# Performance work log

Hardware: AMD Instinct MI355X
Metric: run time of the kernel (lower is better)

The kernel has to match this reference:

```python
import jax, jax.numpy as jnp
import numpy as np

B, S, D_MODEL, N_HEADS = 2, 2048, 1024, 16
HEAD_DIM = D_MODEL // N_HEADS
BASE = 10000.0

# 3D RoPE slice sizes: n_pairs = head_dim//2 split into x,y,z
_n_pairs = HEAD_DIM // 2
_px = _n_pairs // 3
_py = _n_pairs // 3
_pz = _n_pairs - _px - _py
D_X, D_Y, D_Z = _px * 2, _py * 2, _pz * 2  # 20, 20, 24


def _rotate_half(x):
    # interleaved pairs: (x0,x1,x2,x3,...) -> (-x1,x0,-x3,x2,...)
    x1 = x[..., ::2]
    x2 = x[..., 1::2]
    return jnp.stack((-x2, x1), axis=-1).reshape(x.shape)


def _rope_apply(x, pos, dim):
    # x: [B,H,S,dim]; pos: [B,S] int coords
    if dim == 0:
        return x
    inv_freq = 1.0 / (BASE ** (jnp.arange(0, dim, 2, dtype=jnp.float32) / dim))
    t = pos.astype(jnp.float32)[..., None] * inv_freq          # [B,S,dim//2]
    cos = jnp.repeat(jnp.cos(t), 2, axis=-1)[:, None]          # [B,1,S,dim]
    sin = jnp.repeat(jnp.sin(t), 2, axis=-1)[:, None]
    return x * cos + _rotate_half(x) * sin


def _rope3d(q, k, pos_xyz):
    s1, s2, s3 = D_X, D_X + D_Y, D_X + D_Y + D_Z
    parts_q, parts_k = [], []
    for (a, b), ax in (((0, s1), 0), ((s1, s2), 1), ((s2, s3), 2)):
        d = b - a
        parts_q.append(_rope_apply(q[..., a:b], pos_xyz[..., ax], d))
        parts_k.append(_rope_apply(k[..., a:b], pos_xyz[..., ax], d))
    return jnp.concatenate(parts_q, axis=-1), jnp.concatenate(parts_k, axis=-1)


def setup_inputs() -> dict:
    key = jax.random.key(0)
    k1, k2, k3, k4 = jax.random.split(key, 4)
    hidden_states = jax.random.normal(k1, (B, S, D_MODEL), dtype=jnp.float32)
    # padding: each batch row keeps first `len` tokens
    lengths = jnp.array([S - 37, S - 130], dtype=jnp.int32)
    attention_mask = jnp.arange(S)[None, :] < lengths[:, None]          # [B,S] bool, True=keep
    causal_mask = jnp.triu(jnp.ones((S, S), dtype=bool), k=1)[None, None]  # True=masked
    pos_xyz = jax.random.randint(k2, (B, S, 3), 0, 30).astype(jnp.int32)
    w_qkv = jax.random.normal(k3, (3 * D_MODEL, D_MODEL), dtype=jnp.float32) * (D_MODEL ** -0.5)
    w_out = jax.random.normal(k4, (D_MODEL, D_MODEL), dtype=jnp.float32) * (D_MODEL ** -0.5)
    return {"hidden_states": hidden_states, "w_qkv": w_qkv, "w_out": w_out,
            "attention_mask": attention_mask, "causal_mask": causal_mask,
            "pos_xyz": pos_xyz}


def reference(hidden_states, w_qkv, w_out, attention_mask, causal_mask, pos_xyz):
    Bb, Ss, Dd = hidden_states.shape
    scale = HEAD_DIM ** -0.5
    qkv = jnp.einsum('bsd,ed->bse', hidden_states, w_qkv)               # [B,S,3D]
    qkv = qkv.reshape(Bb, Ss, 3, N_HEADS, HEAD_DIM).transpose(2, 0, 3, 1, 4)
    q, k, v = qkv[0], qkv[1], qkv[2]                                    # [B,H,S,hd]
    q, k = _rope3d(q, k, pos_xyz)
    scores = jnp.einsum('bhqd,bhkd->bhqk', q, k) * scale                # [B,H,S,S]
    scores = jnp.where(causal_mask, -jnp.inf, scores)
    scores = jnp.where(attention_mask[:, None, None, :], scores, -jnp.inf)
    weights = jax.nn.softmax(scores, axis=-1)                           # dropout p=0 (eval)
    out = jnp.einsum('bhqk,bhkd->bhqd', weights, v)
    out = out.transpose(0, 2, 1, 3).reshape(Bb, Ss, Dd)
    return jnp.einsum('bsd,ed->bse', out, w_out)
```

## Files before the change

kernel.cpp:

```cpp
#include <hip/hip_runtime.h>
#include <math.h>

extern "C" __device__ float __ocml_native_exp2_f32(float);

namespace {

typedef __attribute__((ext_vector_type(8))) short short8;
typedef __attribute__((ext_vector_type(4))) short short4b;
typedef __attribute__((ext_vector_type(4))) float floatx4;

constexpr int B_ = 2;
constexpr int S_ = 2048;
constexpr int DM_ = 1024;
constexpr int NH_ = 16;
constexpr int HD_ = 64;

__device__ inline unsigned short f2bf(float f) {
  unsigned u = __builtin_bit_cast(unsigned, f);
  u += 0x7fffu + ((u >> 16) & 1u);
  return (unsigned short)(u >> 16);
}

template <int CTRL>
__device__ inline float dpp_ror(float x) {
  const int r = __builtin_amdgcn_update_dpp(
      0, __builtin_bit_cast(int, x), CTRL, 0xF, 0xF, false);
  return __builtin_bit_cast(float, r);
}

__device__ inline void gl2lds16(const unsigned short* g, unsigned short* l) {
  __builtin_amdgcn_global_load_lds(
      (const __attribute__((address_space(1))) unsigned int*)g,
      (__attribute__((address_space(3))) unsigned int*)l, 16, 0, 0);
}

__global__ __launch_bounds__(256) void prep(
    const float* __restrict__ hidden, const float* __restrict__ wqkv,
    const float* __restrict__ wout, const unsigned char* __restrict__ mask,
    unsigned short* __restrict__ hb, int* __restrict__ lengths) {
  const int bid = blockIdx.x;
  if (bid < 4096) {
    const int i = bid * 256 + threadIdx.x;
    const float* src;
    int off;
    if (i < 524288)              { src = hidden; off = 0; }
    else if (i < 524288 + 393216){ src = wqkv;   off = 524288; }
    else                         { src = wout;   off = 524288 + 393216; }
    const size_t j = (size_t)(i - off);
    const float4 a = ((const float4*)src)[j * 2];
    const float4 b = ((const float4*)src)[j * 2 + 1];
    short8 v;
    v[0] = (short)f2bf(a.x); v[1] = (short)f2bf(a.y);
    v[2] = (short)f2bf(a.z); v[3] = (short)f2bf(a.w);
    v[4] = (short)f2bf(b.x); v[5] = (short)f2bf(b.y);
    v[6] = (short)f2bf(b.z); v[7] = (short)f2bf(b.w);
    ((short8*)hb)[i] = v;
  } else {
    const int b = bid - 4096;
    const int es1 = (mask[1] != 0);
    __shared__ int cnt;
    if (threadIdx.x == 0) cnt = 0;
    __syncthreads();
    int local = 0;
    for (int s = threadIdx.x; s < S_; s += blockDim.x) {
      bool nz;
      if (es1) nz = mask[b * S_ + s] != 0;
      else     nz = ((const unsigned int*)mask)[b * S_ + s] != 0;
      local += nz ? 1 : 0;
    }
    atomicAdd(&cnt, local);
    __syncthreads();
    if (threadIdx.x == 0) lengths[b] = cnt;
  }
}

__global__ __launch_bounds__(256) void qkv_gemm(
    const unsigned short* __restrict__ A, const unsigned short* __restrict__ W,
    const int* __restrict__ pos_xyz,
    unsigned short* __restrict__ Qb, unsigned short* __restrict__ Kb,
    unsigned short* __restrict__ Vtb) {
  __shared__ __align__(16) unsigned short As[2][128 * 32];
  __shared__ __align__(16) unsigned short Bs[2][64 * 32];
  const int lin = blockIdx.x;
  const int xcd = lin & 7, t = lin >> 3;
  const int m0 = ((xcd >> 1) * 8 + t / 24) * 128;
  const int n0 = ((xcd & 1) * 24 + t % 24) * 64;
  const int w = threadIdx.x >> 6, lane = threadIdx.x & 63;
  const int lm = lane & 15, q4 = lane >> 4;
  const int srowA = w * 32;
  const int srowB = w * 16;
  const int r_in = lane >> 2;
  const int c_sw = (((lane & 3) ^ ((lane >> 3) & 3)) << 3);
  const int rsw = (lm >> 1) & 3;
  const int wr = (w >> 1) * 64, wc = (w & 1) * 32;
  const int which = n0 >> 10;
  floatx4 acc[8];
  const floatx4 z4 = {0.f, 0.f, 0.f, 0.f};
#pragma unroll
  for (int i = 0; i < 8; i++) acc[i] = z4;

  const unsigned short* gA0 = A + (size_t)(m0 + srowA + r_in) * DM_ + c_sw;
  const unsigned short* gA1 = A + (size_t)(m0 + srowA + 16 + r_in) * DM_ + c_sw;
  const unsigned short* gB0 = W + (size_t)(n0 + srowB + r_in) * DM_ + c_sw;

  for (int k0 = 0; k0 < DM_; k0 += 64) {
#pragma unroll
    for (int hh = 0; hh < 2; hh++) {
      const int ko = k0 + hh * 32;
      gl2lds16(gA0 + ko, As[hh] + srowA * 32);
      gl2lds16(gA1 + ko, As[hh] + (srowA + 16) * 32);
      gl2lds16(gB0 + ko, Bs[hh] + srowB * 32);
    }
    __syncthreads();
#pragma unroll
    for (int hh = 0; hh < 2; hh++) {
      short8 af[4], bf[2];
#pragma unroll
      for (int t2 = 0; t2 < 4; t2++)
        af[t2] = *(const short8*)(As[hh] + (wr + t2 * 16 + lm) * 32 +
                                  ((q4 ^ rsw) << 3));
#pragma unroll
      for (int t2 = 0; t2 < 2; t2++)
        bf[t2] = *(const short8*)(Bs[hh] + (wc + t2 * 16 + lm) * 32 +
                                  ((q4 ^ rsw) << 3));
      if (which == 2) {
#pragma unroll
        for (int i = 0; i < 4; i++)
#pragma unroll
          for (int j = 0; j < 2; j++)
            acc[i * 2 + j] = __builtin_amdgcn_mfma_f32_16x16x32_bf16(
                af[i], bf[j], acc[i * 2 + j], 0, 0, 0);
      } else {
#pragma unroll
        for (int i = 0; i < 2; i++)
#pragma unroll
          for (int j = 0; j < 4; j++)
            acc[i * 4 + j] = __builtin_amdgcn_mfma_f32_16x16x32_bf16(
                bf[i], af[j], acc[i * 4 + j], 0, 0, 0);
      }
    }
    __syncthreads();
  }

  const int h = (n0 & 1023) >> 6;
  if (which == 2) {
#pragma unroll
    for (int nt = 0; nt < 2; nt++) {
      const int d = wc + nt * 16 + lm;
#pragma unroll
      for (int mt = 0; mt < 4; mt++) {
        const int m = m0 + wr + mt * 16 + q4 * 4;
        const int bi = m >> 11, si = m & (S_ - 1);
        short4b pk;
#pragma unroll
        for (int r = 0; r < 4; r++) pk[r] = (short)f2bf(acc[mt * 2 + nt][r]);
        *(short4b*)(Vtb + ((size_t)(bi * NH_ + h) * HD_ + d) * S_ + si) = pk;
      }
    }
  } else {
    unsigned short* Dst = (which == 0) ? Qb : Kb;
    const float osc = (which == 0) ? 0.125f * 1.44269504088896f : 1.0f;
#pragma unroll
    for (int nt = 0; nt < 2; nt++) {
      const int dbase = wc + nt * 16 + q4 * 4;
      const int p0 = dbase >> 1;
      int axis, j0, dseg;
      if (p0 < 10)      { axis = 0; j0 = p0;      dseg = 20; }
      else if (p0 < 20) { axis = 1; j0 = p0 - 10; dseg = 20; }
      else              { axis = 2; j0 = p0 - 20; dseg = 24; }
      const float invf0 =
          __expf(-(2.0f * (float)j0 / (float)dseg) * 9.210340371976184f);
      const float invf1 =
          __expf(-(2.0f * (float)(j0 + 1) / (float)dseg) * 9.210340371976184f);
#pragma unroll
      for (int mt = 0; mt < 4; mt++) {
        const int m = m0 + wr + mt * 16 + lm;
        const int bi = m >> 11, si = m & (S_ - 1);
        const int pos = pos_xyz[((size_t)bi * S_ + si) * 3 + axis];
        short4b pk;
#pragma unroll
        for (int u = 0; u < 2; u++) {
          const float ve = acc[nt * 4 + mt][2 * u];
          const float vo = acc[nt * 4 + mt][2 * u + 1];
          float sn, cs;
          sincosf((float)pos * (u ? invf1 : invf0), &sn, &cs);
          pk[2 * u]     = (short)f2bf(fmaf(ve, cs, -vo * sn) * osc);
          pk[2 * u + 1] = (short)f2bf(fmaf(vo, cs, ve * sn) * osc);
        }
        *(short4b*)(Dst + ((size_t)(bi * NH_ + h) * S_ + si) * HD_ + dbase) = pk;
      }
    }
  }
}

__global__ __launch_bounds__(256) void flash_mfma(
    const unsigned short* __restrict__ Q, const unsigned short* __restrict__ Kg,
    const unsigned short* __restrict__ Vt, const int* __restrict__ lengths,
    unsigned short* __restrict__ Oa) {
  __shared__ __align__(16) unsigned short Ks[2 * 64 * 64];
  __shared__ __align__(16) unsigned short Vs[2 * 64 * 64];
  __shared__ __align__(16) unsigned short Ps[4][16 * 64];

  const int lin = blockIdx.y * gridDim.x + blockIdx.x;
  const int xcd = lin & 7, k = lin >> 3;
  const int s = k >> 5, c = k & 31;
  const int pc = (c & 1) ? 31 - (c >> 1) : (c >> 1);
  const int qt = (s & 1) ? 31 - pc : pc;
  const int bh = xcd * 4 + s;
  const int b = bh >> 4, h = bh & 15;
  const int q0 = qt * 64;

  const int w = threadIdx.x >> 6, lane = threadIdx.x & 63;
  const int lm = lane & 15, q4 = lane >> 4;
  const int len = lengths[b];
  const unsigned short* Qp = Q + (size_t)bh * S_ * HD_;
  const unsigned short* Kp = Kg + (size_t)bh * S_ * HD_;
  const unsigned short* Vp = Vt + (size_t)bh * HD_ * S_;

  const int r8 = lane >> 3, c8 = lane & 7;
  const int rs0 = w * 16 + r8, rs1 = rs0 + 8;
  const int cs = (c8 ^ (rs0 & 7)) << 3;
  const unsigned short* gK0 = Kp + (size_t)rs0 * HD_ + cs;
  const unsigned short* gK1 = Kp + (size_t)rs1 * HD_ + cs;
  const unsigned short* gV0 = Vp + (size_t)rs0 * S_ + cs;
  const unsigned short* gV1 = Vp + (size_t)rs1 * S_ + cs;
  unsigned short* dK0 = Ks + w * 16 * 64;
  unsigned short* dK1 = Ks + (w * 16 + 8) * 64;
  unsigned short* dV0 = Vs + w * 16 * 64;
  unsigned short* dV1 = Vs + (w * 16 + 8) * 64;

  const int qrow = q0 + w * 16 + lm;
  short8 qf[2];
  qf[0] = *(const short8*)(Qp + (size_t)qrow * HD_ + q4 * 8);
  qf[1] = *(const short8*)(Qp + (size_t)qrow * HD_ + 32 + q4 * 8);

  const floatx4 z4 = {0.f, 0.f, 0.f, 0.f};
  floatx4 o[4];
#pragma unroll
  for (int dt = 0; dt < 4; dt++) o[dt] = z4;
  float m_i[4], lp[4];
#pragma unroll
  for (int r = 0; r < 4; r++) { m_i[r] = -1e30f; lp[r] = 0.0f; }

  unsigned short* ps = Ps[w];
  const int ktiles = min(qt + 1, (len + 63) >> 6);

  gl2lds16(gK0, dK0);
  gl2lds16(gK1, dK1);
  gl2lds16(gV0, dV0);
  gl2lds16(gV1, dV1);
  __syncthreads();

  int cur = 0;
  for (int kt = 0; kt < ktiles; kt++) {
    const int k0 = kt * 64;
    if (kt + 1 < ktiles) {
      const size_t koff = (size_t)(k0 + 64) * HD_;
      const int nb = (cur ^ 1) * 4096;
      gl2lds16(gK0 + koff, dK0 + nb);
      gl2lds16(gK1 + koff, dK1 + nb);
      gl2lds16(gV0 + (k0 + 64), dV0 + nb);
      gl2lds16(gV1 + (k0 + 64), dV1 + nb);
    }
    const unsigned short* kc = Ks + cur * 4096;
    const unsigned short* vc = Vs + cur * 4096;

    floatx4 sc[4];
    __builtin_amdgcn_s_setprio(1);
#pragma unroll
    for (int nt = 0; nt < 4; nt++) {
      const int row = nt * 16 + lm, sw = row & 7;
      const unsigned short* kb = kc + row * 64;
      const short8 b0 = *(const short8*)(kb + ((q4 ^ sw) << 3));
      const short8 b1 = *(const short8*)(kb + (((q4 + 4) ^ sw) << 3));
      sc[nt] = __builtin_amdgcn_mfma_f32_16x16x32_bf16(qf[0], b0, z4, 0, 0, 0);
      sc[nt] = __builtin_amdgcn_mfma_f32_16x16x32_bf16(qf[1], b1, sc[nt], 0, 0, 0);
    }
    __builtin_amdgcn_s_setprio(0);
    if (kt == qt || k0 + 64 > len) {
#pragma unroll
      for (int nt = 0; nt < 4; nt++) {
        const int col = k0 + nt * 16 + lm;
#pragma unroll
        for (int r = 0; r < 4; r++) {
          const int row = q0 + w * 16 + q4 * 4 + r;
          if (col > row || col >= len) sc[nt][r] = -1e30f;
        }
      }
    }
    float lmax[4];
#pragma unroll
    for (int r = 0; r < 4; r++)
      lmax[r] = fmaxf(fmaxf(sc[0][r], sc[1][r]), fmaxf(sc[2][r], sc[3][r]));
    const bool ok = (lmax[0] <= m_i[0] + 8.f) && (lmax[1] <= m_i[1] + 8.f) &&
                    (lmax[2] <= m_i[2] + 8.f) && (lmax[3] <= m_i[3] + 8.f);
    if (!__all(ok)) {
#pragma unroll
      for (int r = 0; r < 4; r++) {
        float mx = lmax[r];
        mx = fmaxf(mx, dpp_ror<0x121>(mx));
        mx = fmaxf(mx, dpp_ror<0x122>(mx));
        mx = fmaxf(mx, dpp_ror<0x124>(mx));
        mx = fmaxf(mx, dpp_ror<0x128>(mx));
        const float mt = fmaxf(m_i[r], mx);
        const float al = __ocml_native_exp2_f32(m_i[r] - mt);
        lp[r] *= al;
        m_i[r] = mt;
#pragma unroll
        for (int dt = 0; dt < 4; dt++) o[dt][r] *= al;
      }
    }
#pragma unroll
    for (int r = 0; r < 4; r++) {
      float rs = 0.0f;
#pragma unroll
      for (int nt = 0; nt < 4; nt++) {
        const float pp = __ocml_native_exp2_f32(sc[nt][r] - m_i[r]);
        sc[nt][r] = pp;
        rs += pp;
      }
      lp[r] += rs;
    }
#pragma unroll
    for (int nt = 0; nt < 4; nt++)
#pragma unroll
      for (int r = 0; r < 4; r++) {
        const int row = q4 * 4 + r;
        const int cc = (((nt * 2 + (lm >> 3)) ^ (row & 7)) << 3) | (lm & 7);
        ps[row * 64 + cc] = f2bf(sc[nt][r]);
      }
    __builtin_amdgcn_s_setprio(1);
#pragma unroll
    for (int ks = 0; ks < 2; ks++) {
      const short8 pf = *(const short8*)(
          ps + lm * 64 + ((((ks << 2) + q4) ^ (lm & 7)) << 3));
#pragma unroll
      for (int dt = 0; dt < 4; dt++) {
        const int row = dt * 16 + lm, sw = row & 7;
        const short8 vf = *(const short8*)(
            vc + row * 64 + ((((ks << 2) + q4) ^ sw) << 3));
        o[dt] = __builtin_amdgcn_mfma_f32_16x16x32_bf16(pf, vf, o[dt], 0, 0, 0);
      }
    }
    __builtin_amdgcn_s_setprio(0);
    __syncthreads();
    cur ^= 1;
  }
  float invl[4];
#pragma unroll
  for (int r = 0; r < 4; r++) {
    float l = lp[r];
    l += dpp_ror<0x121>(l);
    l += dpp_ror<0x122>(l);
    l += dpp_ror<0x124>(l);
    l += dpp_ror<0x128>(l);
    invl[r] = 1.0f / l;
  }
#pragma unroll
  for (int dt = 0; dt < 4; dt++)
#pragma unroll
    for (int r = 0; r < 4; r++) {
      const int row = q0 + w * 16 + q4 * 4 + r;
      const int col = h * HD_ + dt * 16 + lm;
      Oa[((size_t)b * S_ + row) * DM_ + col] = f2bf(o[dt][r] * invl[r]);
    }
}

__global__ __launch_bounds__(256) void out_gemm(
    const unsigned short* __restrict__ A, const unsigned short* __restrict__ W,
    float* __restrict__ C) {
  __shared__ __align__(16) unsigned short As[2][64 * 32];
  __shared__ __align__(16) unsigned short Bs[2][64 * 32];
  const int lin = blockIdx.y * gridDim.x + blockIdx.x;
  const int xcd = lin & 7, t = lin >> 3;
  const int m0 = (xcd * 8 + (t >> 4)) * 64;
  const int n0 = (t & 15) * 64;
  const int w = threadIdx.x >> 6, lane = threadIdx.x & 63;
  const int lm = lane & 15, q4 = lane >> 4;
  const int srow = w * 16;
  const int r_in = lane >> 2;
  const int c_sw = (((lane & 3) ^ ((lane >> 3) & 3)) << 3);
  const int rsw = (lm >> 1) & 3;
  const int wr = (w >> 1) * 32, wc = (w & 1) * 32;
  floatx4 acc[2][2];
  const floatx4 z4 = {0.f, 0.f, 0.f, 0.f};
#pragma unroll
  for (int i = 0; i < 2; i++)
#pragma unroll
    for (int j = 0; j < 2; j++) acc[i][j] = z4;

  const unsigned short* gA0 = A + (size_t)(m0 + srow + r_in) * DM_ + c_sw;
  const unsigned short* gB0 = W + (size_t)(n0 + srow + r_in) * DM_ + c_sw;

  for (int k0 = 0; k0 < DM_; k0 += 64) {
#pragma unroll
    for (int hh = 0; hh < 2; hh++) {
      const int ko = k0 + hh * 32;
      gl2lds16(gA0 + ko, As[hh] + srow * 32);
      gl2lds16(gB0 + ko, Bs[hh] + srow * 32);
    }
    __syncthreads();
#pragma unroll
    for (int hh = 0; hh < 2; hh++) {
      short8 af[2], bf[2];
#pragma unroll
      for (int t2 = 0; t2 < 2; t2++)
        af[t2] = *(const short8*)(As[hh] + (wr + t2 * 16 + lm) * 32 +
                                  ((q4 ^ rsw) << 3));
#pragma unroll
      for (int t2 = 0; t2 < 2; t2++)
        bf[t2] = *(const short8*)(Bs[hh] + (wc + t2 * 16 + lm) * 32 +
                                  ((q4 ^ rsw) << 3));
#pragma unroll
      for (int i = 0; i < 2; i++)
#pragma unroll
        for (int j = 0; j < 2; j++)
          acc[i][j] = __builtin_amdgcn_mfma_f32_16x16x32_bf16(
              bf[i], af[j], acc[i][j], 0, 0, 0);
    }
    __syncthreads();
  }
#pragma unroll
  for (int nt = 0; nt < 2; nt++) {
    const int nbase = n0 + wc + nt * 16 + q4 * 4;
#pragma unroll
    for (int mt = 0; mt < 2; mt++) {
      const int m = m0 + wr + mt * 16 + lm;
      *(floatx4*)(C + (size_t)m * DM_ + nbase) = acc[nt][mt];
    }
  }
}

}

extern "C" void kernel_launch(void* const* d_in, const int* in_sizes, int n_in,
                              void* d_out, int out_size, void* d_ws, size_t ws_size,
                              hipStream_t stream) {
  const float* hidden = (const float*)d_in[0];
  const float* w_qkv = (const float*)d_in[1];
  const float* w_out = (const float*)d_in[2];
  const unsigned char* amask = (const unsigned char*)d_in[3];
  const int* pos_xyz = (const int*)d_in[5];
  float* out = (float*)d_out;

  constexpr size_t NHID = (size_t)B_ * S_ * DM_;
  constexpr size_t NWQ = (size_t)3 * DM_ * DM_;
  constexpr size_t NWO = (size_t)DM_ * DM_;
  constexpr size_t NQKV = (size_t)B_ * NH_ * S_ * HD_;

  unsigned short* hb = (unsigned short*)d_ws;
  unsigned short* wqb = hb + NHID;
  unsigned short* wob = wqb + NWQ;
  unsigned short* Qb = wob + NWO;
  unsigned short* Kb = Qb + NQKV;
  unsigned short* Vtb = Kb + NQKV;
  unsigned short* attn = Vtb + NQKV;
  int* lens = (int*)(attn + NQKV);

  prep<<<dim3(4096 + B_), dim3(256), 0, stream>>>(hidden, w_qkv, w_out, amask,
                                                  hb, lens);
  qkv_gemm<<<dim3(1536), dim3(256), 0, stream>>>(hb, wqb, pos_xyz, Qb, Kb,
                                                 Vtb);
  flash_mfma<<<dim3(S_ / 64, B_ * NH_), dim3(256), 0, stream>>>(
      Qb, Kb, Vtb, lens, attn);
  out_gemm<<<dim3(16, 64), dim3(256), 0, stream>>>(attn, wob, out);
}
```

Measured before the change: 210.5 us.

## Double-buffer QKV GEMM LDS tiles with async prefetch of next K slice

The QKV projection GEMM's K loop now uses the two LDS buffers as a ping-pong pair. It prefetches the next 32-wide K slice while computing the current one, using explicit vmcnt waits and raw barriers. Previously both halves were loaded and then waited on fully before computing. The goal is to overlap global-to-LDS load latency with MFMA work, at the cost of twice as many barriers per K step and reliance on manual waitcnt correctness.

```diff
diff --git a/kernel.cpp b/kernel.cpp
--- a/kernel.cpp
+++ b/kernel.cpp
@@ -103,43 +103,49 @@
   const unsigned short* gA1 = A + (size_t)(m0 + srowA + 16 + r_in) * DM_ + c_sw;
   const unsigned short* gB0 = W + (size_t)(n0 + srowB + r_in) * DM_ + c_sw;
 
-  for (int k0 = 0; k0 < DM_; k0 += 64) {
-#pragma unroll
-    for (int hh = 0; hh < 2; hh++) {
-      const int ko = k0 + hh * 32;
-      gl2lds16(gA0 + ko, As[hh] + srowA * 32);
-      gl2lds16(gA1 + ko, As[hh] + (srowA + 16) * 32);
-      gl2lds16(gB0 + ko, Bs[hh] + srowB * 32);
-    }
-    __syncthreads();
-#pragma unroll
-    for (int hh = 0; hh < 2; hh++) {
-      short8 af[4], bf[2];
-#pragma unroll
-      for (int t2 = 0; t2 < 4; t2++)
-        af[t2] = *(const short8*)(As[hh] + (wr + t2 * 16 + lm) * 32 +
-                                  ((q4 ^ rsw) << 3));
-#pragma unroll
-      for (int t2 = 0; t2 < 2; t2++)
-        bf[t2] = *(const short8*)(Bs[hh] + (wc + t2 * 16 + lm) * 32 +
-                                  ((q4 ^ rsw) << 3));
-      if (which == 2) {
-#pragma unroll
-        for (int i = 0; i < 4; i++)
-#pragma unroll
-          for (int j = 0; j < 2; j++)
-            acc[i * 2 + j] = __builtin_amdgcn_mfma_f32_16x16x32_bf16(
-                af[i], bf[j], acc[i * 2 + j], 0, 0, 0);
-      } else {
-#pragma unroll
-        for (int i = 0; i < 2; i++)
-#pragma unroll
-          for (int j = 0; j < 4; j++)
-            acc[i * 4 + j] = __builtin_amdgcn_mfma_f32_16x16x32_bf16(
-                bf[i], af[j], acc[i * 4 + j], 0, 0, 0);
-      }
-    }
-    __syncthreads();
+  gl2lds16(gA0, As[0] + srowA * 32);
+  gl2lds16(gA1, As[0] + (srowA + 16) * 32);
+  gl2lds16(gB0, Bs[0] + srowB * 32);
+
+  int cur = 0;
+  for (int k0 = 0; k0 < DM_; k0 += 32) {
+    if (k0 + 32 < DM_) {
+      const int nb = cur ^ 1;
+      gl2lds16(gA0 + k0 + 32, As[nb] + srowA * 32);
+      gl2lds16(gA1 + k0 + 32, As[nb] + (srowA + 16) * 32);
+      gl2lds16(gB0 + k0 + 32, Bs[nb] + srowB * 32);
+      asm volatile("s_waitcnt vmcnt(3)" ::: "memory");
+    } else {
+      asm volatile("s_waitcnt vmcnt(0)" ::: "memory");
+    }
+    __builtin_amdgcn_s_barrier();
+
+    short8 af[4], bf[2];
+#pragma unroll
+    for (int t2 = 0; t2 < 4; t2++)
+      af[t2] = *(const short8*)(As[cur] + (wr + t2 * 16 + lm) * 32 +
+                                ((q4 ^ rsw) << 3));
+#pragma unroll
+    for (int t2 = 0; t2 < 2; t2++)
+      bf[t2] = *(const short8*)(Bs[cur] + (wc + t2 * 16 + lm) * 32 +
+                                ((q4 ^ rsw) << 3));
+    if (which == 2) {
+#pragma unroll
+      for (int i = 0; i < 4; i++)
+#pragma unroll
+        for (int j = 0; j < 2; j++)
+          acc[i * 2 + j] = __builtin_amdgcn_mfma_f32_16x16x32_bf16(
+              af[i], bf[j], acc[i * 2 + j], 0, 0, 0);
+    } else {
+#pragma unroll
+      for (int i = 0; i < 2; i++)
+#pragma unroll
+        for (int j = 0; j < 4; j++)
+          acc[i * 4 + j] = __builtin_amdgcn_mfma_f32_16x16x32_bf16(
+              bf[i], af[j], acc[i * 4 + j], 0, 0, 0);
+    }
+    __builtin_amdgcn_s_barrier();
+    cur ^= 1;
   }
 
   const int h = (n0 & 1023) >> 6;
```

Result: slower. 217.2 us (+3.2%).

## Double-buffer QKV GEMM shared tiles to overlap global loads with MFMA

Applied to the files above, without the earlier changes.

The QKV projection GEMM gets a second set of LDS tiles so the next K-slice is prefetched via global-to-LDS loads while the current slice is consumed by MFMA. Partial vmcnt waits and raw s_barrier replace the full __syncthreads pairs. This is meant to hide global memory latency in the K loop, at the cost of doubled LDS use (possible occupancy loss) and reliance on manual waitcnt correctness.

```diff
diff --git a/kernel.cpp b/kernel.cpp
--- a/kernel.cpp
+++ b/kernel.cpp
@@ -79,8 +79,8 @@
     const int* __restrict__ pos_xyz,
     unsigned short* __restrict__ Qb, unsigned short* __restrict__ Kb,
     unsigned short* __restrict__ Vtb) {
-  __shared__ __align__(16) unsigned short As[2][128 * 32];
-  __shared__ __align__(16) unsigned short Bs[2][64 * 32];
+  __shared__ __align__(16) unsigned short As[2][2][128 * 32];
+  __shared__ __align__(16) unsigned short Bs[2][2][64 * 32];
   const int lin = blockIdx.x;
   const int xcd = lin & 7, t = lin >> 3;
   const int m0 = ((xcd >> 1) * 8 + t / 24) * 128;
@@ -103,25 +103,42 @@
   const unsigned short* gA1 = A + (size_t)(m0 + srowA + 16 + r_in) * DM_ + c_sw;
   const unsigned short* gB0 = W + (size_t)(n0 + srowB + r_in) * DM_ + c_sw;
 
+#pragma unroll
+  for (int hh = 0; hh < 2; hh++) {
+    const int ko = hh * 32;
+    gl2lds16(gA0 + ko, As[0][hh] + srowA * 32);
+    gl2lds16(gA1 + ko, As[0][hh] + (srowA + 16) * 32);
+    gl2lds16(gB0 + ko, Bs[0][hh] + srowB * 32);
+  }
+
+  int cur = 0;
   for (int k0 = 0; k0 < DM_; k0 += 64) {
-#pragma unroll
-    for (int hh = 0; hh < 2; hh++) {
-      const int ko = k0 + hh * 32;
-      gl2lds16(gA0 + ko, As[hh] + srowA * 32);
-      gl2lds16(gA1 + ko, As[hh] + (srowA + 16) * 32);
-      gl2lds16(gB0 + ko, Bs[hh] + srowB * 32);
-    }
-    __syncthreads();
+    if (k0 + 64 < DM_) {
+      const int nb = cur ^ 1;
+#pragma unroll
+      for (int hh = 0; hh < 2; hh++) {
+        const int ko = k0 + 64 + hh * 32;
+        gl2lds16(gA0 + ko, As[nb][hh] + srowA * 32);
+        gl2lds16(gA1 + ko, As[nb][hh] + (srowA + 16) * 32);
+        gl2lds16(gB0 + ko, Bs[nb][hh] + srowB * 32);
+      }
+      asm volatile("s_waitcnt vmcnt(6)" ::: "memory");
+    } else {
+      asm volatile("s_waitcnt vmcnt(0)" ::: "memory");
+    }
+    __builtin_amdgcn_s_barrier();
+    asm volatile("" ::: "memory");
+
 #pragma unroll
     for (int hh = 0; hh < 2; hh++) {
       short8 af[4], bf[2];
 #pragma unroll
       for (int t2 = 0; t2 < 4; t2++)
-        af[t2] = *(const short8*)(As[hh] + (wr + t2 * 16 + lm) * 32 +
+        af[t2] = *(const short8*)(As[cur][hh] + (wr + t2 * 16 + lm) * 32 +
                                   ((q4 ^ rsw) << 3));
 #pragma unroll
       for (int t2 = 0; t2 < 2; t2++)
-        bf[t2] = *(const short8*)(Bs[hh] + (wc + t2 * 16 + lm) * 32 +
+        bf[t2] = *(const short8*)(Bs[cur][hh] + (wc + t2 * 16 + lm) * 32 +
                                   ((q4 ^ rsw) << 3));
       if (which == 2) {
 #pragma unroll
@@ -139,7 +156,8 @@
                 bf[i], af[j], acc[i * 4 + j], 0, 0, 0);
       }
     }
-    __syncthreads();
+    __builtin_amdgcn_s_barrier();
+    cur ^= 1;
   }
 
   const int h = (n0 & 1023) >> 6;
```

After: 212.5 us. Within noise of the previous version (+1.0%).
